# Kernel optimization log

Measured on AMD Instinct MI355X. Metric: run time of the kernel, lower is better.

Reference implementation:

```python
import jax, jax.numpy as jnp
import numpy as np

DIM = 1024
HEADS = 16
HEAD_DIM = DIM // HEADS
EPS = 1e-5
THETA = 10000.0


def _rope(t):
    # t: (b, s, d). lucidrains rotary: interleaved pairs, full-dim rotation, theta=10000.
    b, s, d = t.shape
    inv_freq = 1.0 / (THETA ** (jnp.arange(0, d, 2, dtype=jnp.float32) / d))  # (d/2,)
    ang = jnp.arange(s, dtype=jnp.float32)[:, None] * inv_freq[None, :]        # (s, d/2)
    cos, sin = jnp.cos(ang), jnp.sin(ang)
    tp = t.reshape(b, s, d // 2, 2)
    x1, x2 = tp[..., 0], tp[..., 1]
    o1 = x1 * cos - x2 * sin
    o2 = x2 * cos + x1 * sin
    return jnp.stack([o1, o2], axis=-1).reshape(b, s, d)


def setup_inputs() -> dict:
    key = jax.random.key(0)
    ks = jax.random.split(key, 10)
    b, s, d = 2, 2048, DIM
    scale = 1.0 / np.sqrt(d)
    return {
        "x": jax.random.normal(ks[0], (b, s, d), dtype=jnp.float32),
        "mask": jax.random.normal(ks[1], (b, s, s), dtype=jnp.float32),
        "ln_g": jnp.ones((d,), dtype=jnp.float32),
        "ln_b": jnp.zeros((d,), dtype=jnp.float32),
        "w_qkv": jax.random.normal(ks[2], (3 * d, d), dtype=jnp.float32) * scale,
        "b_qkv": jnp.zeros((3 * d,), dtype=jnp.float32),
        "in_w": jax.random.normal(ks[3], (3 * d, d), dtype=jnp.float32) * scale,
        "in_b": jnp.zeros((3 * d,), dtype=jnp.float32),
        "out_w": jax.random.normal(ks[4], (d, d), dtype=jnp.float32) * scale,
        "out_b": jnp.zeros((d,), dtype=jnp.float32),
    }


def reference(x, mask, ln_g, ln_b, w_qkv, b_qkv, in_w, in_b, out_w, out_b):
    b, s, d = x.shape
    # LayerNorm
    mu = jnp.mean(x, axis=-1, keepdims=True)
    var = jnp.mean((x - mu) ** 2, axis=-1, keepdims=True)
    xn = (x - mu) * jax.lax.rsqrt(var + EPS) * ln_g + ln_b
    # fused qkv projection, then chunk
    qkv = xn @ w_qkv.T + b_qkv
    q, k, v = jnp.split(qkv, 3, axis=-1)
    # RoPE on q, k (full dim, interleaved pairs)
    q = _rope(q)
    k = _rope(k)
    # nn.MultiheadAttention re-applies its own in-projection
    wq, wk, wv = jnp.split(in_w, 3, axis=0)
    bq, bk, bv = jnp.split(in_b, 3, axis=0)
    def to_heads(t, w, bias):
        t = t @ w.T + bias
        return t.reshape(b, s, HEADS, HEAD_DIM).transpose(0, 2, 1, 3)  # (b,h,s,hd)
    qh = to_heads(q, wq, bq)
    kh = to_heads(k, wk, bk)
    vh = to_heads(v, wv, bv)
    scores = jnp.einsum('bhid,bhjd->bhij', qh, kh) / np.sqrt(HEAD_DIM)
    scores = scores + mask[:, None, :, :]  # mask repeated over heads
    attn = jax.nn.softmax(scores, axis=-1)
    out = jnp.einsum('bhij,bhjd->bhid', attn, vh)
    out = out.transpose(0, 2, 1, 3).reshape(b, s, d)
    return out @ out_w.T + out_b
```

## Files before the change

### kernel.cpp

```cpp
#include <hip/hip_runtime.h>

using u16 = unsigned short;
using u32 = unsigned int;
typedef __attribute__((ext_vector_type(8))) short short8;
typedef __attribute__((ext_vector_type(4))) float f32x4;

#define LOG2E 1.4426950408889634f
#define SCALE2 0.18033688011112042f

__device__ __forceinline__ u16 f2b(float f) {
  union { float f; unsigned u; } v; v.f = f;
  unsigned r = v.u + 0x7fffu + ((v.u >> 16) & 1u);
  return (u16)(r >> 16);
}

typedef const __attribute__((address_space(1))) u32* gp_t;
typedef __attribute__((address_space(3))) u32* lp_t;
__device__ __forceinline__ void gl_lds16(const u16* g, u16* l) {
  __builtin_amdgcn_global_load_lds((gp_t)g, (lp_t)l, 16, 0, 0);
}

__global__ __launch_bounds__(256) void prep(const float* __restrict__ w_qkv, u16* __restrict__ wqkv_b,
                                            const float* __restrict__ in_w, u16* __restrict__ inw_b,
                                            const float* __restrict__ out_w, u16* __restrict__ outw_b,
                                            float2* __restrict__ rtab,
                                            const float* __restrict__ mask, u16* __restrict__ maskp) {
  __shared__ u16 T[128 * 68];
  int blk = blockIdx.x, t = threadIdx.x;
  if (blk < 7168) {
    int i = blk * 256 + t;
    const float* s; u16* d; int off;
    if (i < 786432)       { s = w_qkv; d = wqkv_b; off = i; }
    else if (i < 1572864) { s = in_w;  d = inw_b;  off = i - 786432; }
    else                  { s = out_w; d = outw_b; off = i - 1572864; }
    float4 v = ((const float4*)s)[off];
    uint2 o;
    o.x = (unsigned)f2b(v.x) | ((unsigned)f2b(v.y) << 16);
    o.y = (unsigned)f2b(v.z) | ((unsigned)f2b(v.w) << 16);
    ((uint2*)d)[off] = o;
  } else if (blk < 11264) {
    int idx = (blk - 7168) * 256 + t;
    int pos = idx >> 9, i = idx & 511;
    float ifreq = exp2f(-(float)(2 * i) * (13.287712379549449f / 1024.0f));
    float ang = (float)pos * ifreq;
    rtab[idx] = make_float2(__cosf(ang), __sinf(ang));
  } else {
    int mb = blk - 11264;
    int kt = mb & 31, qt = (mb >> 5) & 15, bb = mb >> 9;
    const float* src = mask + ((size_t)bb * 2048 + qt * 128) * 2048 + kt * 64;
    #pragma unroll
    for (int it = 0; it < 8; it++) {
      int id = it * 256 + t;
      int r = id >> 4, c4 = (id & 15) * 4;
      float4 v = *(const float4*)(src + (size_t)r * 2048 + c4);
      T[r * 68 + c4 + 0] = f2b(v.x * LOG2E);
      T[r * 68 + c4 + 1] = f2b(v.y * LOG2E);
      T[r * 68 + c4 + 2] = f2b(v.z * LOG2E);
      T[r * 68 + c4 + 3] = f2b(v.w * LOG2E);
    }
    __syncthreads();
    size_t obase = (size_t)(((bb * 16 + qt) * 32) + kt) * 8192;
    #pragma unroll
    for (int it = 0; it < 2; it++) {
      int pos = it * 256 + t;
      int l15 = pos & 15, g = pos >> 4;
      int w = g >> 3, p = (g >> 2) & 1, qd = g & 3;
      int qlocal = w * 32 + p * 16 + l15;
      u16 vals[16];
      #pragma unroll
      for (int mt = 0; mt < 4; mt++)
        #pragma unroll
        for (int reg = 0; reg < 4; reg++)
          vals[mt * 4 + reg] = T[qlocal * 68 + mt * 16 + qd * 4 + reg];
      uint4* dst = (uint4*)(maskp + obase + (size_t)pos * 16);
      dst[0] = *(uint4*)&vals[0];
      dst[1] = *(uint4*)&vals[8];
    }
  }
}

__global__ __launch_bounds__(256) void ln_pack(const float* __restrict__ x,
                                               const float* __restrict__ g,
                                               const float* __restrict__ beta,
                                               u16* __restrict__ xn) {
  int row = blockIdx.x;
  int t = threadIdx.x;
  const float* xr = x + (size_t)row * 1024;
  float4 v = *(const float4*)(xr + t * 4);
  float s = v.x + v.y + v.z + v.w;
  float ss = v.x * v.x + v.y * v.y + v.z * v.z + v.w * v.w;
  #pragma unroll
  for (int m = 1; m < 64; m <<= 1) {
    s  += __shfl_xor(s, m);
    ss += __shfl_xor(ss, m);
  }
  __shared__ float sbuf[4], ssbuf[4];
  int wave = t >> 6, lane = t & 63;
  if (lane == 0) { sbuf[wave] = s; ssbuf[wave] = ss; }
  __syncthreads();
  s  = sbuf[0] + sbuf[1] + sbuf[2] + sbuf[3];
  ss = ssbuf[0] + ssbuf[1] + ssbuf[2] + ssbuf[3];
  float mean = s * (1.0f / 1024.0f);
  float var  = ss * (1.0f / 1024.0f) - mean * mean;
  float rstd = 1.0f / sqrtf(var + 1e-5f);
  float4 gv = *(const float4*)(g + t * 4);
  float4 bv = *(const float4*)(beta + t * 4);
  uint2 o;
  o.x = (unsigned)f2b((v.x - mean) * rstd * gv.x + bv.x) |
        ((unsigned)f2b((v.y - mean) * rstd * gv.y + bv.y) << 16);
  o.y = (unsigned)f2b((v.z - mean) * rstd * gv.z + bv.z) |
        ((unsigned)f2b((v.w - mean) * rstd * gv.w + bv.w) << 16);
  *(uint2*)(xn + (size_t)row * 1024 + t * 4) = o;
}

template<bool SLAB, bool OUT_BF16, bool ROPE>
__global__ __launch_bounds__(256) void gemm_mfma(const u16* __restrict__ A, int lda,
                                                 const u16* __restrict__ W,
                                                 const float* __restrict__ bias,
                                                 const float2* __restrict__ rtab,
                                                 float* __restrict__ Cf,
                                                 u16* __restrict__ Cb,
                                                 int ldc, int K) {
  __shared__ u16 As[128 * 64];
  __shared__ u16 Bs[128 * 64];
  int n0 = blockIdx.x * 128, m0 = blockIdx.y * 128;
  int aoff = SLAB ? ((n0 >> 10) << 10) : 0;
  int tid = threadIdx.x;
  int lane = tid & 63, l15 = lane & 15, quad = lane >> 4;
  int w = tid >> 6, mw = w & 1, nw = w >> 1;
  const u16* Abase = A + (size_t)m0 * lda + aoff;
  const u16* Wbase = W + (size_t)n0 * K;
  int lrow = lane >> 3, lcol = (lane & 7) * 8;
  f32x4 acc[4][4];
  #pragma unroll
  for (int i = 0; i < 4; i++)
    #pragma unroll
    for (int j = 0; j < 4; j++) acc[i][j] = (f32x4){0.f, 0.f, 0.f, 0.f};

  for (int k0 = 0; k0 < K; k0 += 64) {
    __syncthreads();
    #pragma unroll
    for (int c = 0; c < 4; c++) {
      int row = c * 32 + w * 8 + lrow;
      gl_lds16(Abase + (size_t)row * lda + k0 + lcol, &As[(c * 32 + w * 8) * 64]);
      gl_lds16(Wbase + (size_t)row * K   + k0 + lcol, &Bs[(c * 32 + w * 8) * 64]);
    }
    __syncthreads();
    #pragma unroll
    for (int kk = 0; kk < 64; kk += 32) {
      short8 af[4], bfr[4];
      #pragma unroll
      for (int mt = 0; mt < 4; mt++)
        af[mt] = *(const short8*)&As[(mw * 64 + mt * 16 + l15) * 64 + kk + quad * 8];
      #pragma unroll
      for (int nt = 0; nt < 4; nt++)
        bfr[nt] = *(const short8*)&Bs[(nw * 64 + nt * 16 + l15) * 64 + kk + quad * 8];
      #pragma unroll
      for (int mt = 0; mt < 4; mt++)
        #pragma unroll
        for (int nt = 0; nt < 4; nt++)
          acc[mt][nt] = __builtin_amdgcn_mfma_f32_16x16x32_bf16(
              af[mt], bfr[nt], acc[mt][nt], 0, 0, 0);
    }
  }
  int mb = m0 + mw * 64, nb = n0 + nw * 64;
  float bv[4];
  #pragma unroll
  for (int nt = 0; nt < 4; nt++) bv[nt] = bias[nb + nt * 16 + l15];
  #pragma unroll
  for (int mt = 0; mt < 4; mt++)
    #pragma unroll
    for (int nt = 0; nt < 4; nt++) {
      int col = nb + nt * 16 + l15;
      #pragma unroll
      for (int reg = 0; reg < 4; reg++) {
        int row = mb + mt * 16 + quad * 4 + reg;
        float val = acc[mt][nt][reg] + bv[nt];
        if (ROPE && col < 2048) {
          float pr = __shfl_xor(val, 1);
          float2 cs = rtab[(size_t)(row & 2047) * 512 + ((col & 1023) >> 1)];
          val = (col & 1) ? fmaf(val, cs.x, pr * cs.y)
                          : fmaf(val, cs.x, -pr * cs.y);
        }
        if (OUT_BF16) Cb[(size_t)row * ldc + col] = f2b(val);
        else          Cf[(size_t)row * ldc + col] = val;
      }
    }
}

__global__ __launch_bounds__(256) void transpose_v(const u16* __restrict__ qkv2,
                                                   u16* __restrict__ vT) {
  __shared__ u16 T[64 * 72];
  int st = blockIdx.x, h = blockIdx.y, bb = blockIdx.z;
  int t = threadIdx.x;
  int r = t >> 2, c0 = (t & 3) * 16;
  const u16* src = qkv2 + (size_t)(bb * 2048 + st * 64 + r) * 3072 + 2048 + h * 64 + c0;
  *(uint4*)&T[r * 72 + c0]     = *(const uint4*)src;
  *(uint4*)&T[r * 72 + c0 + 8] = *(const uint4*)(src + 8);
  __syncthreads();
  int d = t >> 2, s0 = (t & 3) * 16;
  u16 tmp[16];
  #pragma unroll
  for (int j = 0; j < 16; j++) tmp[j] = T[(s0 + j) * 72 + d];
  u16* dst = vT + ((size_t)((bb * 16 + h) * 64 + d)) * 2048 + st * 64 + s0;
  *(uint4*)dst       = *(uint4*)&tmp[0];
  *(uint4*)(dst + 8) = *(uint4*)&tmp[8];
}

__global__ __launch_bounds__(256) void attn_mfma(const u16* __restrict__ qkv2,
                                                 const u16* __restrict__ vT,
                                                 const u16* __restrict__ maskp,
                                                 u16* __restrict__ attn_out) {
  __shared__ u16 Kb[2][64 * 72];
  __shared__ u16 Vb[2][64 * 72];
  __shared__ u16 Ps[128 * 72];
  int h = blockIdx.x, qt = blockIdx.y, bb = blockIdx.z;
  int tid = threadIdx.x;
  int lane = tid & 63, l15 = lane & 15, quad = lane >> 4;
  int w = tid >> 6;
  int sr = tid >> 2, sc = (tid & 3) * 16;
  const u16* kslab = qkv2 + ((size_t)bb * 2048) * 3072 + 1024 + h * 64;
  const u16* vslab = vT + ((size_t)((bb * 16 + h) * 64)) * 2048;

  {
    int r = w * 32 + (lane >> 1), c0 = (lane & 1) * 32;
    const u16* src = qkv2 + (size_t)(bb * 2048 + qt * 128 + r) * 3072 + h * 64 + c0;
    #pragma unroll
    for (int u = 0; u < 4; u++)
      *(uint4*)&Ps[r * 72 + c0 + u * 8] = *(const uint4*)(src + u * 8);
  }
  {
    const u16* ks = kslab + (size_t)sr * 3072 + sc;
    const u16* vs = vslab + (size_t)sr * 2048 + sc;
    *(uint4*)&Kb[0][sr * 72 + sc]     = *(const uint4*)ks;
    *(uint4*)&Kb[0][sr * 72 + sc + 8] = *(const uint4*)(ks + 8);
    *(uint4*)&Vb[0][sr * 72 + sc]     = *(const uint4*)vs;
    *(uint4*)&Vb[0][sr * 72 + sc + 8] = *(const uint4*)(vs + 8);
  }
  short8 bq[2][2];
  #pragma unroll
  for (int p = 0; p < 2; p++)
    #pragma unroll
    for (int hk = 0; hk < 2; hk++)
      bq[p][hk] = *(const short8*)&Ps[(w * 32 + p * 16 + l15) * 72 + hk * 32 + quad * 8];
  float lsum[2] = {0.f, 0.f};
  f32x4 acc[2][4];
  #pragma unroll
  for (int p = 0; p < 2; p++)
    #pragma unroll
    for (int dt = 0; dt < 4; dt++) acc[p][dt] = (f32x4){0.f, 0.f, 0.f, 0.f};
  const u16* mtile = maskp + ((size_t)((bb * 16 + qt) * 32)) * 8192
                     + (((w * 2) * 4 + quad) * 16 + l15) * 16;
  __syncthreads();

  for (int kt = 0; kt < 32; kt++) {
    int b = kt & 1;
    uint4 mA[2], mB[2];
    {
      const u16* mt_ = mtile + (size_t)kt * 8192;
      #pragma unroll
      for (int p = 0; p < 2; p++) {
        const uint4* mq = (const uint4*)(mt_ + p * 1024);
        mA[p] = mq[0]; mB[p] = mq[1];
      }
    }
    uint4 kr0, kr1, vr0, vr1;
    if (kt + 1 < 32) {
      const u16* ks = kslab + (size_t)((kt + 1) * 64 + sr) * 3072 + sc;
      const u16* vs = vslab + (size_t)sr * 2048 + (kt + 1) * 64 + sc;
      kr0 = *(const uint4*)ks; kr1 = *(const uint4*)(ks + 8);
      vr0 = *(const uint4*)vs; vr1 = *(const uint4*)(vs + 8);
    }
    short8 ak[4][2];
    #pragma unroll
    for (int mt = 0; mt < 4; mt++)
      #pragma unroll
      for (int hk = 0; hk < 2; hk++)
        ak[mt][hk] = *(const short8*)&Kb[b][(mt * 16 + l15) * 72 + hk * 32 + quad * 8];
    #pragma unroll
    for (int p = 0; p < 2; p++) {
      f32x4 st[4];
      #pragma unroll
      for (int mt = 0; mt < 4; mt++) {
        f32x4 z = (f32x4){0.f, 0.f, 0.f, 0.f};
        z = __builtin_amdgcn_mfma_f32_16x16x32_bf16(ak[mt][0], bq[p][0], z, 0, 0, 0);
        st[mt] = __builtin_amdgcn_mfma_f32_16x16x32_bf16(ak[mt][1], bq[p][1], z, 0, 0, 0);
      }
      u32 wds[8] = {mA[p].x, mA[p].y, mA[p].z, mA[p].w, mB[p].x, mB[p].y, mB[p].z, mB[p].w};
      float mv[16];
      #pragma unroll
      for (int j = 0; j < 8; j++) {
        mv[2 * j]     = __uint_as_float(wds[j] << 16);
        mv[2 * j + 1] = __uint_as_float(wds[j] & 0xffff0000u);
      }
      int prow = (w * 32 + p * 16 + l15) * 72 + quad * 4;
      #pragma unroll
      for (int mt = 0; mt < 4; mt++) {
        u32 pk0, pk1;
        float sv0 = fmaf(st[mt][0], SCALE2, mv[mt * 4 + 0]);
        float sv1 = fmaf(st[mt][1], SCALE2, mv[mt * 4 + 1]);
        float sv2 = fmaf(st[mt][2], SCALE2, mv[mt * 4 + 2]);
        float sv3 = fmaf(st[mt][3], SCALE2, mv[mt * 4 + 3]);
        float p0 = __builtin_amdgcn_exp2f(sv0), p1 = __builtin_amdgcn_exp2f(sv1);
        float p2 = __builtin_amdgcn_exp2f(sv2), p3 = __builtin_amdgcn_exp2f(sv3);
        lsum[p] += (p0 + p1) + (p2 + p3);
        pk0 = ((__float_as_uint(p0) + 0x8000u) >> 16) |
              ((__float_as_uint(p1) + 0x8000u) & 0xffff0000u);
        pk1 = ((__float_as_uint(p2) + 0x8000u) >> 16) |
              ((__float_as_uint(p3) + 0x8000u) & 0xffff0000u);
        *(uint2*)&Ps[prow + mt * 16] = make_uint2(pk0, pk1);
      }
    }
    short8 ap[2][2];
    #pragma unroll
    for (int p = 0; p < 2; p++)
      #pragma unroll
      for (int hk = 0; hk < 2; hk++)
        ap[p][hk] = *(const short8*)&Ps[(w * 32 + p * 16 + l15) * 72 + hk * 32 + quad * 8];
    #pragma unroll
    for (int dt = 0; dt < 4; dt++) {
      short8 bv0 = *(const short8*)&Vb[b][(dt * 16 + l15) * 72 + quad * 8];
      short8 bv1 = *(const short8*)&Vb[b][(dt * 16 + l15) * 72 + 32 + quad * 8];
      #pragma unroll
      for (int p = 0; p < 2; p++) {
        acc[p][dt] = __builtin_amdgcn_mfma_f32_16x16x32_bf16(ap[p][0], bv0, acc[p][dt], 0, 0, 0);
        acc[p][dt] = __builtin_amdgcn_mfma_f32_16x16x32_bf16(ap[p][1], bv1, acc[p][dt], 0, 0, 0);
      }
    }
    if (kt + 1 < 32) {
      int nb = b ^ 1;
      *(uint4*)&Kb[nb][sr * 72 + sc]     = kr0;
      *(uint4*)&Kb[nb][sr * 72 + sc + 8] = kr1;
      *(uint4*)&Vb[nb][sr * 72 + sc]     = vr0;
      *(uint4*)&Vb[nb][sr * 72 + sc + 8] = vr1;
    }
    __syncthreads();
  }
  #pragma unroll
  for (int p = 0; p < 2; p++) {
    float l = lsum[p];
    l += __shfl_xor(l, 16);
    l += __shfl_xor(l, 32);
    #pragma unroll
    for (int reg = 0; reg < 4; reg++) {
      float lq = __shfl(l, quad * 4 + reg);
      float inv = 1.0f / lq;
      int grow = bb * 2048 + qt * 128 + w * 32 + p * 16 + quad * 4 + reg;
      #pragma unroll
      for (int dt = 0; dt < 4; dt++)
        attn_out[(size_t)grow * 1024 + h * 64 + dt * 16 + l15] = f2b(acc[p][dt][reg] * inv);
    }
  }
}

extern "C" void kernel_launch(void* const* d_in, const int* in_sizes, int n_in,
                              void* d_out, int out_size, void* d_ws, size_t ws_size,
                              hipStream_t stream) {
  const float* x     = (const float*)d_in[0];
  const float* mask  = (const float*)d_in[1];
  const float* ln_g  = (const float*)d_in[2];
  const float* ln_b  = (const float*)d_in[3];
  const float* w_qkv = (const float*)d_in[4];
  const float* b_qkv = (const float*)d_in[5];
  const float* in_w  = (const float*)d_in[6];
  const float* in_b  = (const float*)d_in[7];
  const float* out_w = (const float*)d_in[8];
  const float* out_b = (const float*)d_in[9];
  float* out = (float*)d_out;
  char* ws = (char*)d_ws;

  u16* wqkv_b = (u16*)(ws);
  u16* inw_b  = (u16*)(ws + 6291456ull);
  u16* outw_b = (u16*)(ws + 12582912ull);
  u16* xn_b   = (u16*)(ws + 14680064ull);
  u16* attn_b = xn_b;
  u16* qkv_b  = (u16*)(ws + 23068672ull);
  u16* qkv2_b = (u16*)(ws + 48234496ull);
  float2* rtab = (float2*)qkv2_b;
  u16* vT     = (u16*)(ws + 73400320ull);
  u16* maskp  = (u16*)(ws + 81788928ull);

  prep<<<12288, 256, 0, stream>>>(w_qkv, wqkv_b, in_w, inw_b, out_w, outw_b,
                                  rtab, mask, maskp);
  ln_pack<<<4096, 256, 0, stream>>>(x, ln_g, ln_b, xn_b);
  gemm_mfma<false, true, true><<<dim3(24, 32), 256, 0, stream>>>(
      xn_b, 1024, wqkv_b, b_qkv, rtab, nullptr, qkv_b, 3072, 1024);
  gemm_mfma<true, true, false><<<dim3(24, 32), 256, 0, stream>>>(
      qkv_b, 3072, inw_b, in_b, nullptr, nullptr, qkv2_b, 3072, 1024);
  transpose_v<<<dim3(32, 16, 2), 256, 0, stream>>>(qkv2_b, vT);
  attn_mfma<<<dim3(16, 16, 2), 256, 0, stream>>>(qkv2_b, vT, maskp, attn_b);
  gemm_mfma<false, false, false><<<dim3(8, 32), 256, 0, stream>>>(
      attn_b, 1024, outw_b, out_b, nullptr, out, nullptr, 1024, 1024);
}
```

Before: 355.2 us.

## Double-buffer GEMM tiles via register prefetch and pad LDS rows

Replaces the direct global-to-LDS loads in the MFMA GEMM with register-staged loads into a double-buffered LDS tile. The next K-slice is fetched into registers while MFMAs run on the current buffer, then stored to the other buffer, which leaves one barrier per iteration. Rows are padded from 64 to 72 elements to reduce LDS bank conflicts on fragment reads. This doubles LDS use and adds register pressure, which can lower occupancy.

New measurement: 493.4 us. +38.9%, slower.

```diff
diff --git a/kernel.cpp b/kernel.cpp
--- a/kernel.cpp
+++ b/kernel.cpp
@@ -12,12 +12,6 @@
   union { float f; unsigned u; } v; v.f = f;
   unsigned r = v.u + 0x7fffu + ((v.u >> 16) & 1u);
   return (u16)(r >> 16);
-}
-
-typedef const __attribute__((address_space(1))) u32* gp_t;
-typedef __attribute__((address_space(3))) u32* lp_t;
-__device__ __forceinline__ void gl_lds16(const u16* g, u16* l) {
-  __builtin_amdgcn_global_load_lds((gp_t)g, (lp_t)l, 16, 0, 0);
 }
 
 __global__ __launch_bounds__(256) void prep(const float* __restrict__ w_qkv, u16* __restrict__ wqkv_b,
@@ -121,8 +115,8 @@
                                                  float* __restrict__ Cf,
                                                  u16* __restrict__ Cb,
                                                  int ldc, int K) {
-  __shared__ u16 As[128 * 64];
-  __shared__ u16 Bs[128 * 64];
+  __shared__ u16 As[2][128 * 72];
+  __shared__ u16 Bs[2][128 * 72];
   int n0 = blockIdx.x * 128, m0 = blockIdx.y * 128;
   int aoff = SLAB ? ((n0 >> 10) << 10) : 0;
   int tid = threadIdx.x;
@@ -130,31 +124,50 @@
   int w = tid >> 6, mw = w & 1, nw = w >> 1;
   const u16* Abase = A + (size_t)m0 * lda + aoff;
   const u16* Wbase = W + (size_t)n0 * K;
-  int lrow = lane >> 3, lcol = (lane & 7) * 8;
   f32x4 acc[4][4];
   #pragma unroll
   for (int i = 0; i < 4; i++)
     #pragma unroll
     for (int j = 0; j < 4; j++) acc[i][j] = (f32x4){0.f, 0.f, 0.f, 0.f};
 
+  uint4 ar[4], wr[4];
+  #define GLOAD(k0)                                                         \
+    {                                                                       \
+      _Pragma("unroll")                                                     \
+      for (int c = 0; c < 4; c++) {                                         \
+        int idx = c * 256 + tid;                                            \
+        int row = idx >> 3, c8 = (idx & 7) * 8;                             \
+        ar[c] = *(const uint4*)(Abase + (size_t)row * lda + (k0) + c8);     \
+        wr[c] = *(const uint4*)(Wbase + (size_t)row * K + (k0) + c8);       \
+      }                                                                     \
+    }
+  #define LSTORE(b)                                                         \
+    {                                                                       \
+      _Pragma("unroll")                                                     \
+      for (int c = 0; c < 4; c++) {                                         \
+        int idx = c * 256 + tid;                                            \
+        int row = idx >> 3, c8 = (idx & 7) * 8;                             \
+        *(uint4*)&As[b][row * 72 + c8] = ar[c];                             \
+        *(uint4*)&Bs[b][row * 72 + c8] = wr[c];                             \
+      }                                                                     \
+    }
+
+  GLOAD(0);
+  LSTORE(0);
+  __syncthreads();
   for (int k0 = 0; k0 < K; k0 += 64) {
-    __syncthreads();
-    #pragma unroll
-    for (int c = 0; c < 4; c++) {
-      int row = c * 32 + w * 8 + lrow;
-      gl_lds16(Abase + (size_t)row * lda + k0 + lcol, &As[(c * 32 + w * 8) * 64]);
-      gl_lds16(Wbase + (size_t)row * K   + k0 + lcol, &Bs[(c * 32 + w * 8) * 64]);
-    }
-    __syncthreads();
+    int b = (k0 >> 6) & 1;
+    bool more = (k0 + 64 < K);
+    if (more) GLOAD(k0 + 64);
     #pragma unroll
     for (int kk = 0; kk < 64; kk += 32) {
       short8 af[4], bfr[4];
       #pragma unroll
       for (int mt = 0; mt < 4; mt++)
-        af[mt] = *(const short8*)&As[(mw * 64 + mt * 16 + l15) * 64 + kk + quad * 8];
+        af[mt] = *(const short8*)&As[b][(mw * 64 + mt * 16 + l15) * 72 + kk + quad * 8];
       #pragma unroll
       for (int nt = 0; nt < 4; nt++)
-        bfr[nt] = *(const short8*)&Bs[(nw * 64 + nt * 16 + l15) * 64 + kk + quad * 8];
+        bfr[nt] = *(const short8*)&Bs[b][(nw * 64 + nt * 16 + l15) * 72 + kk + quad * 8];
       #pragma unroll
       for (int mt = 0; mt < 4; mt++)
         #pragma unroll
@@ -162,6 +175,8 @@
           acc[mt][nt] = __builtin_amdgcn_mfma_f32_16x16x32_bf16(
               af[mt], bfr[nt], acc[mt][nt], 0, 0, 0);
     }
+    if (more) LSTORE(b ^ 1);
+    __syncthreads();
   }
   int mb = m0 + mw * 64, nb = n0 + nw * 64;
   float bv[4];
```

## Double-buffer GEMM tiles through registers and fold LayerNorm into prep kernel

Applied to the files above, without the earlier changes.

The GEMM kernel replaces direct global-to-LDS loads with register-staged loads into double-buffered, padded (stride 72) LDS tiles. The next tile is prefetched into registers while the current one is computed, so each k-step needs one barrier instead of two. LayerNorm is merged into the prep kernel as extra blocks, removing one launch. The trade-off is higher register pressure, twice the LDS, and a launch-bounds occupancy hint of 2.

Measured after the change: 321.1 us. 9.6% less time.

```diff
diff --git a/kernel.cpp b/kernel.cpp
--- a/kernel.cpp
+++ b/kernel.cpp
@@ -14,18 +14,17 @@
   return (u16)(r >> 16);
 }
 
-typedef const __attribute__((address_space(1))) u32* gp_t;
-typedef __attribute__((address_space(3))) u32* lp_t;
-__device__ __forceinline__ void gl_lds16(const u16* g, u16* l) {
-  __builtin_amdgcn_global_load_lds((gp_t)g, (lp_t)l, 16, 0, 0);
-}
-
 __global__ __launch_bounds__(256) void prep(const float* __restrict__ w_qkv, u16* __restrict__ wqkv_b,
                                             const float* __restrict__ in_w, u16* __restrict__ inw_b,
                                             const float* __restrict__ out_w, u16* __restrict__ outw_b,
                                             float2* __restrict__ rtab,
-                                            const float* __restrict__ mask, u16* __restrict__ maskp) {
+                                            const float* __restrict__ mask, u16* __restrict__ maskp,
+                                            const float* __restrict__ x,
+                                            const float* __restrict__ ln_g,
+                                            const float* __restrict__ ln_b,
+                                            u16* __restrict__ xn) {
   __shared__ u16 T[128 * 68];
+  __shared__ float sbuf[4], ssbuf[4];
   int blk = blockIdx.x, t = threadIdx.x;
   if (blk < 7168) {
     int i = blk * 256 + t;
@@ -44,7 +43,7 @@
     float ifreq = exp2f(-(float)(2 * i) * (13.287712379549449f / 1024.0f));
     float ang = (float)pos * ifreq;
     rtab[idx] = make_float2(__cosf(ang), __sinf(ang));
-  } else {
+  } else if (blk < 12288) {
     int mb = blk - 11264;
     int kt = mb & 31, qt = (mb >> 5) & 15, bb = mb >> 9;
     const float* src = mask + ((size_t)bb * 2048 + qt * 128) * 2048 + kt * 64;
@@ -76,53 +75,46 @@
       dst[0] = *(uint4*)&vals[0];
       dst[1] = *(uint4*)&vals[8];
     }
-  }
-}
-
-__global__ __launch_bounds__(256) void ln_pack(const float* __restrict__ x,
-                                               const float* __restrict__ g,
-                                               const float* __restrict__ beta,
-                                               u16* __restrict__ xn) {
-  int row = blockIdx.x;
-  int t = threadIdx.x;
-  const float* xr = x + (size_t)row * 1024;
-  float4 v = *(const float4*)(xr + t * 4);
-  float s = v.x + v.y + v.z + v.w;
-  float ss = v.x * v.x + v.y * v.y + v.z * v.z + v.w * v.w;
-  #pragma unroll
-  for (int m = 1; m < 64; m <<= 1) {
-    s  += __shfl_xor(s, m);
-    ss += __shfl_xor(ss, m);
-  }
-  __shared__ float sbuf[4], ssbuf[4];
-  int wave = t >> 6, lane = t & 63;
-  if (lane == 0) { sbuf[wave] = s; ssbuf[wave] = ss; }
-  __syncthreads();
-  s  = sbuf[0] + sbuf[1] + sbuf[2] + sbuf[3];
-  ss = ssbuf[0] + ssbuf[1] + ssbuf[2] + ssbuf[3];
-  float mean = s * (1.0f / 1024.0f);
-  float var  = ss * (1.0f / 1024.0f) - mean * mean;
-  float rstd = 1.0f / sqrtf(var + 1e-5f);
-  float4 gv = *(const float4*)(g + t * 4);
-  float4 bv = *(const float4*)(beta + t * 4);
-  uint2 o;
-  o.x = (unsigned)f2b((v.x - mean) * rstd * gv.x + bv.x) |
-        ((unsigned)f2b((v.y - mean) * rstd * gv.y + bv.y) << 16);
-  o.y = (unsigned)f2b((v.z - mean) * rstd * gv.z + bv.z) |
-        ((unsigned)f2b((v.w - mean) * rstd * gv.w + bv.w) << 16);
-  *(uint2*)(xn + (size_t)row * 1024 + t * 4) = o;
+  } else {
+    int row = blk - 12288;
+    const float* xr = x + (size_t)row * 1024;
+    float4 v = *(const float4*)(xr + t * 4);
+    float s = v.x + v.y + v.z + v.w;
+    float ss = v.x * v.x + v.y * v.y + v.z * v.z + v.w * v.w;
+    #pragma unroll
+    for (int m = 1; m < 64; m <<= 1) {
+      s  += __shfl_xor(s, m);
+      ss += __shfl_xor(ss, m);
+    }
+    int wave = t >> 6, lane = t & 63;
+    if (lane == 0) { sbuf[wave] = s; ssbuf[wave] = ss; }
+    __syncthreads();
+    s  = sbuf[0] + sbuf[1] + sbuf[2] + sbuf[3];
+    ss = ssbuf[0] + ssbuf[1] + ssbuf[2] + ssbuf[3];
+    float mean = s * (1.0f / 1024.0f);
+    float var  = ss * (1.0f / 1024.0f) - mean * mean;
+    float rstd = 1.0f / sqrtf(var + 1e-5f);
+    float4 gv = *(const float4*)(ln_g + t * 4);
+    float4 bv = *(const float4*)(ln_b + t * 4);
+    uint2 o;
+    o.x = (unsigned)f2b((v.x - mean) * rstd * gv.x + bv.x) |
+          ((unsigned)f2b((v.y - mean) * rstd * gv.y + bv.y) << 16);
+    o.y = (unsigned)f2b((v.z - mean) * rstd * gv.z + bv.z) |
+          ((unsigned)f2b((v.w - mean) * rstd * gv.w + bv.w) << 16);
+    *(uint2*)(xn + (size_t)row * 1024 + t * 4) = o;
+  }
 }
 
 template<bool SLAB, bool OUT_BF16, bool ROPE>
-__global__ __launch_bounds__(256) void gemm_mfma(const u16* __restrict__ A, int lda,
-                                                 const u16* __restrict__ W,
-                                                 const float* __restrict__ bias,
-                                                 const float2* __restrict__ rtab,
-                                                 float* __restrict__ Cf,
-                                                 u16* __restrict__ Cb,
-                                                 int ldc, int K) {
-  __shared__ u16 As[128 * 64];
-  __shared__ u16 Bs[128 * 64];
+__global__ __launch_bounds__(256, 2) void gemm_pipe(const u16* __restrict__ A, int lda,
+                                                    const u16* __restrict__ W,
+                                                    const float* __restrict__ bias,
+                                                    const float2* __restrict__ rtab,
+                                                    float* __restrict__ Cf,
+                                                    u16* __restrict__ Cb,
+                                                    int ldc, int K) {
+  __shared__ u16 As[2][128 * 72];
+  __shared__ u16 Bs[2][128 * 72];
   int n0 = blockIdx.x * 128, m0 = blockIdx.y * 128;
   int aoff = SLAB ? ((n0 >> 10) << 10) : 0;
   int tid = threadIdx.x;
@@ -130,31 +122,51 @@
   int w = tid >> 6, mw = w & 1, nw = w >> 1;
   const u16* Abase = A + (size_t)m0 * lda + aoff;
   const u16* Wbase = W + (size_t)n0 * K;
-  int lrow = lane >> 3, lcol = (lane & 7) * 8;
+  int r0 = tid >> 3;
+  int c8 = (tid & 7) * 8;
   f32x4 acc[4][4];
   #pragma unroll
   for (int i = 0; i < 4; i++)
     #pragma unroll
     for (int j = 0; j < 4; j++) acc[i][j] = (f32x4){0.f, 0.f, 0.f, 0.f};
 
+  uint4 a0, a1, a2, a3, w0, w1, w2, w3;
+  #define GLOADS(k0)                                                          \
+    a0 = *(const uint4*)(Abase + (size_t)(r0)      * lda + (k0) + c8);        \
+    a1 = *(const uint4*)(Abase + (size_t)(r0 + 32) * lda + (k0) + c8);        \
+    a2 = *(const uint4*)(Abase + (size_t)(r0 + 64) * lda + (k0) + c8);        \
+    a3 = *(const uint4*)(Abase + (size_t)(r0 + 96) * lda + (k0) + c8);        \
+    w0 = *(const uint4*)(Wbase + (size_t)(r0)      * K   + (k0) + c8);        \
+    w1 = *(const uint4*)(Wbase + (size_t)(r0 + 32) * K   + (k0) + c8);        \
+    w2 = *(const uint4*)(Wbase + (size_t)(r0 + 64) * K   + (k0) + c8);        \
+    w3 = *(const uint4*)(Wbase + (size_t)(r0 + 96) * K   + (k0) + c8);
+  #define LSTORES(b)                                                          \
+    *(uint4*)&As[b][(r0)      * 72 + c8] = a0;                                \
+    *(uint4*)&As[b][(r0 + 32) * 72 + c8] = a1;                                \
+    *(uint4*)&As[b][(r0 + 64) * 72 + c8] = a2;                                \
+    *(uint4*)&As[b][(r0 + 96) * 72 + c8] = a3;                                \
+    *(uint4*)&Bs[b][(r0)      * 72 + c8] = w0;                                \
+    *(uint4*)&Bs[b][(r0 + 32) * 72 + c8] = w1;                                \
+    *(uint4*)&Bs[b][(r0 + 64) * 72 + c8] = w2;                                \
+    *(uint4*)&Bs[b][(r0 + 96) * 72 + c8] = w3;
+
+  GLOADS(0);
+  LSTORES(0);
+  if (K > 64) { GLOADS(64); }
+  __syncthreads();
   for (int k0 = 0; k0 < K; k0 += 64) {
-    __syncthreads();
-    #pragma unroll
-    for (int c = 0; c < 4; c++) {
-      int row = c * 32 + w * 8 + lrow;
-      gl_lds16(Abase + (size_t)row * lda + k0 + lcol, &As[(c * 32 + w * 8) * 64]);
-      gl_lds16(Wbase + (size_t)row * K   + k0 + lcol, &Bs[(c * 32 + w * 8) * 64]);
-    }
-    __syncthreads();
+    int b = (k0 >> 6) & 1;
+    if (k0 + 64 < K)  { LSTORES(b ^ 1); }
+    if (k0 + 128 < K) { GLOADS(k0 + 128); }
     #pragma unroll
     for (int kk = 0; kk < 64; kk += 32) {
       short8 af[4], bfr[4];
       #pragma unroll
       for (int mt = 0; mt < 4; mt++)
-        af[mt] = *(const short8*)&As[(mw * 64 + mt * 16 + l15) * 64 + kk + quad * 8];
+        af[mt] = *(const short8*)&As[b][(mw * 64 + mt * 16 + l15) * 72 + kk + quad * 8];
       #pragma unroll
       for (int nt = 0; nt < 4; nt++)
-        bfr[nt] = *(const short8*)&Bs[(nw * 64 + nt * 16 + l15) * 64 + kk + quad * 8];
+        bfr[nt] = *(const short8*)&Bs[b][(nw * 64 + nt * 16 + l15) * 72 + kk + quad * 8];
       #pragma unroll
       for (int mt = 0; mt < 4; mt++)
         #pragma unroll
@@ -162,7 +174,10 @@
           acc[mt][nt] = __builtin_amdgcn_mfma_f32_16x16x32_bf16(
               af[mt], bfr[nt], acc[mt][nt], 0, 0, 0);
     }
-  }
+    __syncthreads();
+  }
+  #undef GLOADS
+  #undef LSTORES
   int mb = m0 + mw * 64, nb = n0 + nw * 64;
   float bv[4];
   #pragma unroll
@@ -380,15 +395,14 @@
   u16* vT     = (u16*)(ws + 73400320ull);
   u16* maskp  = (u16*)(ws + 81788928ull);
 
-  prep<<<12288, 256, 0, stream>>>(w_qkv, wqkv_b, in_w, inw_b, out_w, outw_b,
-                                  rtab, mask, maskp);
-  ln_pack<<<4096, 256, 0, stream>>>(x, ln_g, ln_b, xn_b);
-  gemm_mfma<false, true, true><<<dim3(24, 32), 256, 0, stream>>>(
+  prep<<<16384, 256, 0, stream>>>(w_qkv, wqkv_b, in_w, inw_b, out_w, outw_b,
+                                  rtab, mask, maskp, x, ln_g, ln_b, xn_b);
+  gemm_pipe<false, true, true><<<dim3(24, 32), 256, 0, stream>>>(
       xn_b, 1024, wqkv_b, b_qkv, rtab, nullptr, qkv_b, 3072, 1024);
-  gemm_mfma<true, true, false><<<dim3(24, 32), 256, 0, stream>>>(
+  gemm_pipe<true, true, false><<<dim3(24, 32), 256, 0, stream>>>(
       qkv_b, 3072, inw_b, in_b, nullptr, nullptr, qkv2_b, 3072, 1024);
   transpose_v<<<dim3(32, 16, 2), 256, 0, stream>>>(qkv2_b, vT);
   attn_mfma<<<dim3(16, 16, 2), 256, 0, stream>>>(qkv2_b, vT, maskp, attn_b);
-  gemm_mfma<false, false, false><<<dim3(8, 32), 256, 0, stream>>>(
+  gemm_pipe<false, false, false><<<dim3(8, 32), 256, 0, stream>>>(
       attn_b, 1024, outw_b, out_b, nullptr, out, nullptr, 1024, 1024);
 }
```
